# Kernel optimization log

Measured on AMD Instinct MI355X. Metric: run time of the kernel, lower is better.

Reference implementation:

```python
import jax, jax.numpy as jnp
import numpy as np

OUT_FEAT = 11008
IN_FEAT = 4096
HAD_DIM = 128


def setup_inputs() -> dict:
    key = jax.random.key(0)
    k1, k2, k3 = jax.random.split(key, 3)
    inp = jax.random.normal(k1, (OUT_FEAT, IN_FEAT), dtype=jnp.float32) * 0.02
    # rotation matrices (Hadamard-like random orthogonal stand-ins, scaled)
    R_left = jax.random.normal(k2, (IN_FEAT, IN_FEAT), dtype=jnp.float32) / np.sqrt(IN_FEAT)
    R_right = jax.random.normal(k3, (HAD_DIM, HAD_DIM), dtype=jnp.float32) / np.sqrt(HAD_DIM)
    return {"inp": inp, "R_left": R_left, "R_right": R_right}


def _fake_quant_int8(x):
    # symmetric per-tensor int8 fake quant with straight-through estimator
    scale = jnp.max(jnp.abs(x)) / 127.0
    scale = jnp.maximum(scale, jnp.finfo(x.dtype).tiny)
    q = jnp.clip(jnp.round(x / scale), -127.0, 127.0) * scale
    return x + jax.lax.stop_gradient(q - x)


def reference(inp, R_left, R_right):
    # RotQuantWrapper.forward, branch: R_left is not None, R1_is_left=True, R_right set.
    org_dtype = inp.dtype
    out_feat, in_feat = inp.shape  # inp is W^T: (out_feat, in_feat)
    compute_dtype = jnp.float32
    # inp @ R_left  -> (out_feat, in_feat)
    x = inp.astype(compute_dtype) @ R_left.astype(compute_dtype)
    had_dim = R_right.shape[0]
    # (W^T A)^T -> reshape -> block-multiply by B (had_dim blocks) -> back
    x = x.T  # (in_feat, out_feat)
    x = x.reshape(in_feat, out_feat // had_dim, had_dim)
    x = x @ R_right.astype(compute_dtype)  # batched small matmul over 128-blocks
    x = x.reshape(in_feat, out_feat).T  # (out_feat, in_feat)
    x = x.astype(org_dtype)
    return _fake_quant_int8(x)
```

## Files before the change

kernel.cpp:

```cpp
#include <hip/hip_runtime.h>

#define OUT_FEAT 11008
#define IN_FEAT  4096
#define HAD      128

typedef __attribute__((ext_vector_type(8))) _Float16 f16x8;
typedef __attribute__((ext_vector_type(4))) float    f32x4;

__device__ __forceinline__ void lds_load16(const _Float16* g, _Float16* l) {
    __builtin_amdgcn_global_load_lds(
        (const __attribute__((address_space(1))) void*)g,
        (__attribute__((address_space(3))) void*)l, 16, 0, 0);
}

__global__ void k_transpose_convert(const float* __restrict__ Rl, _Float16* __restrict__ Bt) {
    __shared__ float tile[64][65];
    int n0 = blockIdx.x * 64;
    int k0 = blockIdx.y * 64;
    int t  = threadIdx.x;
    int tn = t & 63;
    int tr = t >> 6;
#pragma unroll
    for (int r = 0; r < 16; ++r) {
        int kk = r * 4 + tr;
        tile[kk][tn] = Rl[(size_t)(k0 + kk) * IN_FEAT + n0 + tn];
    }
    __syncthreads();
#pragma unroll
    for (int r = 0; r < 16; ++r) {
        int nn = r * 4 + tr;
        Bt[(size_t)(n0 + nn) * IN_FEAT + k0 + tn] = (_Float16)tile[tn][nn];
    }
}

__global__ __launch_bounds__(256, 1) void k_rotate(const float* __restrict__ inp,
                                                   const float* __restrict__ Rr,
                                                   _Float16* __restrict__ W) {
    __shared__ float sR[HAD * HAD];
    __shared__ float sX[HAD * 128];
    int i0 = blockIdx.x * 128;
    int b  = blockIdx.y;
    int t  = threadIdx.x;

    for (int r = 0; r < 64; ++r) {
        int idx = r * 256 + t;
        sR[idx] = Rr[idx];
    }
    const float* xsrc = inp + (size_t)b * HAD * IN_FEAT + i0;
    for (int r = 0; r < 64; ++r) {
        int idx = r * 256 + t;
        int k = idx >> 7, ii = idx & 127;
        sX[idx] = xsrc[(size_t)k * IN_FEAT + ii];
    }
    __syncthreads();

    int tx = t & 15, ty = t >> 4;
    int j0 = ty * 8, ii0 = tx * 8;
    float acc[8][8];
#pragma unroll
    for (int a = 0; a < 8; ++a)
#pragma unroll
        for (int c = 0; c < 8; ++c) acc[a][c] = 0.f;

    for (int k = 0; k < 128; ++k) {
        float4 ra = *(const float4*)&sR[k * 128 + j0];
        float4 rb = *(const float4*)&sR[k * 128 + j0 + 4];
        float4 xa = *(const float4*)&sX[k * 128 + ii0];
        float4 xb = *(const float4*)&sX[k * 128 + ii0 + 4];
        float rv[8] = {ra.x, ra.y, ra.z, ra.w, rb.x, rb.y, rb.z, rb.w};
        float xv[8] = {xa.x, xa.y, xa.z, xa.w, xb.x, xb.y, xb.z, xb.w};
#pragma unroll
        for (int jj = 0; jj < 8; ++jj)
#pragma unroll
            for (int ii = 0; ii < 8; ++ii)
                acc[jj][ii] = fmaf(rv[jj], xv[ii], acc[jj][ii]);
    }

#pragma unroll
    for (int jj = 0; jj < 8; ++jj) {
        f16x8 v;
#pragma unroll
        for (int ii = 0; ii < 8; ++ii) v[ii] = (_Float16)acc[jj][ii];
        *(f16x8*)&W[(size_t)(b * HAD + j0 + jj) * IN_FEAT + i0 + ii0] = v;
    }
}

#define BM 256
#define BN 256
#define BK 32
#define NT (IN_FEAT / BK)

__global__ __launch_bounds__(512, 2) void k_gemm(const _Float16* __restrict__ A,
                                                 const _Float16* __restrict__ B,
                                                 float* __restrict__ C,
                                                 unsigned* __restrict__ absmax) {
    __shared__ _Float16 sA[4][BM * BK];
    __shared__ _Float16 sB[4][BN * BK];

    int obid = blockIdx.x;
    int cpx  = 688 >> 3;
    int bid  = (obid & 7) * cpx + (obid >> 3);
    int m0 = (bid >> 4) * BM;
    int n0 = (bid & 15) * BN;

    int t    = threadIdx.x;
    int lane = t & 63;
    int wid  = t >> 6;
    int wr   = wid >> 2;
    int wc   = wid & 3;

    int pc0 = t;
    int pc1 = t + 512;
    int rowP0 = pc0 >> 2, rowP1 = pc1 >> 2;
    int csw0 = ((pc0 & 3) ^ ((pc0 >> 3) & 3)) * 8;
    int csw1 = ((pc1 & 3) ^ ((pc1 >> 3) & 3)) * 8;
    const _Float16* A0 = A + (size_t)(m0 + rowP0) * IN_FEAT + csw0;
    const _Float16* A1 = A + (size_t)(m0 + rowP1) * IN_FEAT + csw1;
    const _Float16* B0 = B + (size_t)(n0 + rowP0) * IN_FEAT + csw0;
    const _Float16* B1 = B + (size_t)(n0 + rowP1) * IN_FEAT + csw1;
    int ldsOff0 = (wid * 64) * 8;
    int ldsOff1 = (512 + wid * 64) * 8;

    auto stageA = [&](int s, int kt) {
        lds_load16(A0 + kt * BK, &sA[s][ldsOff0]);
        lds_load16(A1 + kt * BK, &sA[s][ldsOff1]);
    };
    auto stageB = [&](int s, int kt) {
        lds_load16(B0 + kt * BK, &sB[s][ldsOff0]);
        lds_load16(B1 + kt * BK, &sB[s][ldsOff1]);
    };

    int fr  = lane & 15;
    int fc8 = (((lane >> 4) ^ ((lane >> 1) & 3))) * 8;
    int aoff0 = (wr * 128 + fr) * BK + fc8;
    int aoff1 = (wr * 128 + 64 + fr) * BK + fc8;
    int boff  = (wc * 64 + fr) * BK + fc8;

    f32x4 acc[8][4] = {};
    f16x8 af[4], bf[4];

    stageA(0, 0); stageB(0, 0);
    stageA(1, 1); stageB(1, 1);
    asm volatile("s_waitcnt vmcnt(4)" ::: "memory");
    __builtin_amdgcn_s_barrier();

    for (int kt = 0; kt < NT; ++kt) {
        int s  = kt & 3;
        int sn = (kt + 2) & 3;
        bool st = (kt + 2) < NT;

        const _Float16* pa = &sA[s][aoff0];
        const _Float16* pb = &sB[s][boff];
#pragma unroll
        for (int i = 0; i < 4; ++i) bf[i] = *(const f16x8*)(pb + i * 16 * BK);
#pragma unroll
        for (int i = 0; i < 4; ++i) af[i] = *(const f16x8*)(pa + i * 16 * BK);
        if (st) stageA(sn, kt + 2);
        __builtin_amdgcn_s_barrier();
        __builtin_amdgcn_s_setprio(1);
#pragma unroll
        for (int mi = 0; mi < 4; ++mi)
#pragma unroll
            for (int ni = 0; ni < 4; ++ni)
                acc[mi][ni] = __builtin_amdgcn_mfma_f32_16x16x32_f16(af[mi], bf[ni], acc[mi][ni], 0, 0, 0);
        __builtin_amdgcn_s_setprio(0);
        __builtin_amdgcn_s_barrier();

        const _Float16* pa1 = &sA[s][aoff1];
#pragma unroll
        for (int i = 0; i < 4; ++i) af[i] = *(const f16x8*)(pa1 + i * 16 * BK);
        if (st) stageB(sn, kt + 2);
        __builtin_amdgcn_s_barrier();
        __builtin_amdgcn_s_setprio(1);
#pragma unroll
        for (int mi = 0; mi < 4; ++mi)
#pragma unroll
            for (int ni = 0; ni < 4; ++ni)
                acc[4 + mi][ni] = __builtin_amdgcn_mfma_f32_16x16x32_f16(af[mi], bf[ni], acc[4 + mi][ni], 0, 0, 0);
        __builtin_amdgcn_s_setprio(0);
        if (st) asm volatile("s_waitcnt vmcnt(4)" ::: "memory");
        else    asm volatile("s_waitcnt vmcnt(0)" ::: "memory");
        __builtin_amdgcn_s_barrier();
    }

    float mx = 0.f;
#pragma unroll
    for (int mi = 0; mi < 8; ++mi)
#pragma unroll
        for (int ni = 0; ni < 4; ++ni)
#pragma unroll
            for (int r = 0; r < 4; ++r) mx = fmaxf(mx, fabsf(acc[mi][ni][r]));
#pragma unroll
    for (int off = 32; off; off >>= 1) mx = fmaxf(mx, __shfl_xor(mx, off));
    if (lane == 0) atomicMax(absmax, __float_as_uint(mx));

#pragma unroll
    for (int mi = 0; mi < 8; ++mi) {
        int row_base = m0 + wr * 128 + mi * 16 + (lane >> 4) * 4;
#pragma unroll
        for (int ni = 0; ni < 4; ++ni) {
            int col = n0 + wc * 64 + ni * 16 + (lane & 15);
#pragma unroll
            for (int r = 0; r < 4; ++r)
                C[(size_t)(row_base + r) * IN_FEAT + col] = acc[mi][ni][r];
        }
    }
}

__global__ void k_quant(float* __restrict__ C, const unsigned* __restrict__ absmax, int n4) {
    int i = blockIdx.x * blockDim.x + threadIdx.x;
    if (i >= n4) return;
    float amax  = __uint_as_float(*absmax);
    float scale = fmaxf(amax / 127.0f, 1.17549435e-38f);
    float4 v = ((const float4*)C)[i];
    float4 o;
    o.x = fminf(127.f, fmaxf(-127.f, rintf(v.x / scale))) * scale;
    o.y = fminf(127.f, fmaxf(-127.f, rintf(v.y / scale))) * scale;
    o.z = fminf(127.f, fmaxf(-127.f, rintf(v.z / scale))) * scale;
    o.w = fminf(127.f, fmaxf(-127.f, rintf(v.w / scale))) * scale;
    ((float4*)C)[i] = o;
}

extern "C" void kernel_launch(void* const* d_in, const int* in_sizes, int n_in,
                              void* d_out, int out_size, void* d_ws, size_t ws_size,
                              hipStream_t stream) {
    const float* inp = (const float*)d_in[0];
    const float* Rl  = (const float*)d_in[1];
    const float* Rr  = (const float*)d_in[2];
    float* out = (float*)d_out;

    char* ws = (char*)d_ws;
    const size_t W_BYTES  = (size_t)OUT_FEAT * IN_FEAT * 2;
    const size_t BT_BYTES = (size_t)IN_FEAT * IN_FEAT * 2;
    _Float16* Wh   = (_Float16*)ws;
    _Float16* Bt   = (_Float16*)(ws + W_BYTES);
    unsigned* amax = (unsigned*)(ws + W_BYTES + BT_BYTES);

    hipMemsetAsync(amax, 0, 4, stream);
    k_transpose_convert<<<dim3(IN_FEAT / 64, IN_FEAT / 64), 256, 0, stream>>>(Rl, Bt);
    k_rotate<<<dim3(IN_FEAT / 128, OUT_FEAT / HAD), 256, 0, stream>>>(inp, Rr, Wh);
    k_gemm<<<dim3((OUT_FEAT / BM) * (IN_FEAT / BN)), 512, 0, stream>>>(Wh, Bt, out, amax);
    int n4 = OUT_FEAT * IN_FEAT / 4;
    k_quant<<<(n4 + 255) / 256, 256, 0, stream>>>(out, amax, n4);
}
```

Measured before the change: 699.3 us.

## Restructure GEMM main loop to BK=64 with half-tile staged double buffering

Raises the GEMM K-tile from 32 to 64 and splits each A/B tile into 128-row halves staged separately into LDS. The loop becomes four MFMA phases per K-step, each interleaved with one half-tile async load. Loads are ordered A one step ahead and B two steps ahead, with a new XOR swizzle for 64-wide rows. The aim is to halve loop iterations and barriers per unit of work and to overlap global-to-LDS traffic with MFMA better. In exchange it adds more barriers per iteration and tighter buffer-reuse hazards, and LDS use stays at 128KB per block.

```diff
diff --git a/kernel.cpp b/kernel.cpp
--- a/kernel.cpp
+++ b/kernel.cpp
@@ -87,99 +87,125 @@
 
 #define BM 256
 #define BN 256
-#define BK 32
+#define BK 64
 #define NT (IN_FEAT / BK)
 
 __global__ __launch_bounds__(512, 2) void k_gemm(const _Float16* __restrict__ A,
                                                  const _Float16* __restrict__ B,
                                                  float* __restrict__ C,
                                                  unsigned* __restrict__ absmax) {
-    __shared__ _Float16 sA[4][BM * BK];
-    __shared__ _Float16 sB[4][BN * BK];
+    __shared__ _Float16 sA[4 * 8192];
+    __shared__ _Float16 sB[4 * 8192];
 
     int obid = blockIdx.x;
-    int cpx  = 688 >> 3;
-    int bid  = (obid & 7) * cpx + (obid >> 3);
+    int bid  = (obid & 7) * 86 + (obid >> 3);
     int m0 = (bid >> 4) * BM;
     int n0 = (bid & 15) * BN;
 
-    int t    = threadIdx.x;
-    int lane = t & 63;
-    int wid  = t >> 6;
-    int wr   = wid >> 2;
-    int wc   = wid & 3;
-
-    int pc0 = t;
-    int pc1 = t + 512;
-    int rowP0 = pc0 >> 2, rowP1 = pc1 >> 2;
-    int csw0 = ((pc0 & 3) ^ ((pc0 >> 3) & 3)) * 8;
-    int csw1 = ((pc1 & 3) ^ ((pc1 >> 3) & 3)) * 8;
-    const _Float16* A0 = A + (size_t)(m0 + rowP0) * IN_FEAT + csw0;
-    const _Float16* A1 = A + (size_t)(m0 + rowP1) * IN_FEAT + csw1;
-    const _Float16* B0 = B + (size_t)(n0 + rowP0) * IN_FEAT + csw0;
-    const _Float16* B1 = B + (size_t)(n0 + rowP1) * IN_FEAT + csw1;
-    int ldsOff0 = (wid * 64) * 8;
-    int ldsOff1 = (512 + wid * 64) * 8;
-
-    auto stageA = [&](int s, int kt) {
-        lds_load16(A0 + kt * BK, &sA[s][ldsOff0]);
-        lds_load16(A1 + kt * BK, &sA[s][ldsOff1]);
+    int t = threadIdx.x, lane = t & 63, wid = t >> 6;
+    int wr = wid >> 2, wc = wid & 3;
+    int fr = lane & 15, g = lane >> 4;
+
+    int r0 = t >> 3,        r1 = (t + 512) >> 3;
+    int cs0 = ((t & 7) ^ (r0 & 7)) * 8;
+    int cs1 = (((t + 512) & 7) ^ (r1 & 7)) * 8;
+    size_t sOff0 = (size_t)r0 * IN_FEAT + cs0;
+    size_t sOff1 = (size_t)r1 * IN_FEAT + cs1;
+    const _Float16* Abase = A + (size_t)m0 * IN_FEAT;
+    const _Float16* Bbase = B + (size_t)n0 * IN_FEAT;
+    int d0 = (wid * 64) * 8;
+    int d1 = (512 + wid * 64) * 8;
+
+    auto stA = [&](int bufi, int h, int ktc) {
+        const _Float16* s = Abase + (size_t)(h * 128) * IN_FEAT + ktc * BK;
+        _Float16* d = &sA[(bufi * 2 + h) * 8192];
+        lds_load16(s + sOff0, d + d0);
+        lds_load16(s + sOff1, d + d1);
     };
-    auto stageB = [&](int s, int kt) {
-        lds_load16(B0 + kt * BK, &sB[s][ldsOff0]);
-        lds_load16(B1 + kt * BK, &sB[s][ldsOff1]);
+    auto stB = [&](int bufi, int h, int ktc) {
+        const _Float16* s = Bbase + (size_t)(h * 128) * IN_FEAT + ktc * BK;
+        _Float16* d = &sB[(bufi * 2 + h) * 8192];
+        lds_load16(s + sOff0, d + d0);
+        lds_load16(s + sOff1, d + d1);
     };
 
-    int fr  = lane & 15;
-    int fc8 = (((lane >> 4) ^ ((lane >> 1) & 3))) * 8;
-    int aoff0 = (wr * 128 + fr) * BK + fc8;
-    int aoff1 = (wr * 128 + 64 + fr) * BK + fc8;
-    int boff  = (wc * 64 + fr) * BK + fc8;
+    int pk0 = ((g) ^ (fr & 7)) * 8;
+    int pk1 = (((4 | g)) ^ (fr & 7)) * 8;
+    int aRow = fr * 64;
+    int bRow = (wc & 1) * 4096 + fr * 64;
 
     f32x4 acc[8][4] = {};
-    f16x8 af[4], bf[4];
-
-    stageA(0, 0); stageB(0, 0);
-    stageA(1, 1); stageB(1, 1);
+    f16x8 a[4], b0[4], b1[4];
+
+    stB(0, 0, 0); stB(0, 1, 0);
+    stA(0, 0, 0); stA(0, 1, 0);
+    stB(1, 0, 1); stB(1, 1, 1);
     asm volatile("s_waitcnt vmcnt(4)" ::: "memory");
     __builtin_amdgcn_s_barrier();
 
     for (int kt = 0; kt < NT; ++kt) {
-        int s  = kt & 3;
-        int sn = (kt + 2) & 3;
-        bool st = (kt + 2) < NT;
-
-        const _Float16* pa = &sA[s][aoff0];
-        const _Float16* pb = &sB[s][boff];
-#pragma unroll
-        for (int i = 0; i < 4; ++i) bf[i] = *(const f16x8*)(pb + i * 16 * BK);
-#pragma unroll
-        for (int i = 0; i < 4; ++i) af[i] = *(const f16x8*)(pa + i * 16 * BK);
-        if (st) stageA(sn, kt + 2);
-        __builtin_amdgcn_s_barrier();
-        __builtin_amdgcn_s_setprio(1);
-#pragma unroll
-        for (int mi = 0; mi < 4; ++mi)
-#pragma unroll
-            for (int ni = 0; ni < 4; ++ni)
-                acc[mi][ni] = __builtin_amdgcn_mfma_f32_16x16x32_f16(af[mi], bf[ni], acc[mi][ni], 0, 0, 0);
-        __builtin_amdgcn_s_setprio(0);
-        __builtin_amdgcn_s_barrier();
-
-        const _Float16* pa1 = &sA[s][aoff1];
-#pragma unroll
-        for (int i = 0; i < 4; ++i) af[i] = *(const f16x8*)(pa1 + i * 16 * BK);
-        if (st) stageB(sn, kt + 2);
-        __builtin_amdgcn_s_barrier();
-        __builtin_amdgcn_s_setprio(1);
-#pragma unroll
-        for (int mi = 0; mi < 4; ++mi)
-#pragma unroll
-            for (int ni = 0; ni < 4; ++ni)
-                acc[4 + mi][ni] = __builtin_amdgcn_mfma_f32_16x16x32_f16(af[mi], bf[ni], acc[4 + mi][ni], 0, 0, 0);
-        __builtin_amdgcn_s_setprio(0);
-        if (st) asm volatile("s_waitcnt vmcnt(4)" ::: "memory");
-        else    asm volatile("s_waitcnt vmcnt(0)" ::: "memory");
+        int buf = kt & 1, nb = buf ^ 1;
+        const _Float16* sa = &sA[(buf * 2 + wr) * 8192 + aRow];
+        const _Float16* sb = &sB[(buf * 2 + (wc >> 1)) * 8192 + bRow];
+        bool ok1 = (kt + 1) < NT;
+        bool ok2 = (kt + 2) < NT;
+
+#pragma unroll
+        for (int i = 0; i < 4; ++i) a[i]  = *(const f16x8*)(sa + i * 1024 + pk0);
+#pragma unroll
+        for (int i = 0; i < 4; ++i) b0[i] = *(const f16x8*)(sb + i * 1024 + pk0);
+        if (ok1) stA(nb, 0, kt + 1);
+        __builtin_amdgcn_s_barrier();
+        __builtin_amdgcn_s_setprio(1);
+#pragma unroll
+        for (int mi = 0; mi < 4; ++mi)
+#pragma unroll
+            for (int ni = 0; ni < 4; ++ni)
+                acc[mi][ni] = __builtin_amdgcn_mfma_f32_16x16x32_f16(a[mi], b0[ni], acc[mi][ni], 0, 0, 0);
+        __builtin_amdgcn_s_setprio(0);
+        __builtin_amdgcn_s_barrier();
+
+#pragma unroll
+        for (int i = 0; i < 4; ++i) a[i]  = *(const f16x8*)(sa + i * 1024 + pk1);
+#pragma unroll
+        for (int i = 0; i < 4; ++i) b1[i] = *(const f16x8*)(sb + i * 1024 + pk1);
+        if (ok1) stA(nb, 1, kt + 1);
+        __builtin_amdgcn_s_barrier();
+        __builtin_amdgcn_s_setprio(1);
+#pragma unroll
+        for (int mi = 0; mi < 4; ++mi)
+#pragma unroll
+            for (int ni = 0; ni < 4; ++ni)
+                acc[mi][ni] = __builtin_amdgcn_mfma_f32_16x16x32_f16(a[mi], b1[ni], acc[mi][ni], 0, 0, 0);
+        __builtin_amdgcn_s_setprio(0);
+        __builtin_amdgcn_s_barrier();
+
+#pragma unroll
+        for (int i = 0; i < 4; ++i) a[i] = *(const f16x8*)(sa + (4 + i) * 1024 + pk0);
+        if (ok2) stB(buf, 0, kt + 2);
+        __builtin_amdgcn_s_barrier();
+        __builtin_amdgcn_s_setprio(1);
+#pragma unroll
+        for (int mi = 0; mi < 4; ++mi)
+#pragma unroll
+            for (int ni = 0; ni < 4; ++ni)
+                acc[4 + mi][ni] = __builtin_amdgcn_mfma_f32_16x16x32_f16(a[mi], b0[ni], acc[4 + mi][ni], 0, 0, 0);
+        __builtin_amdgcn_s_setprio(0);
+        __builtin_amdgcn_s_barrier();
+
+#pragma unroll
+        for (int i = 0; i < 4; ++i) a[i] = *(const f16x8*)(sa + (4 + i) * 1024 + pk1);
+        if (ok2) stB(buf, 1, kt + 2);
+        __builtin_amdgcn_s_barrier();
+        __builtin_amdgcn_s_setprio(1);
+#pragma unroll
+        for (int mi = 0; mi < 4; ++mi)
+#pragma unroll
+            for (int ni = 0; ni < 4; ++ni)
+                acc[4 + mi][ni] = __builtin_amdgcn_mfma_f32_16x16x32_f16(a[mi], b1[ni], acc[4 + mi][ni], 0, 0, 0);
+        __builtin_amdgcn_s_setprio(0);
+        if (ok2) asm volatile("s_waitcnt vmcnt(4)" ::: "memory");
+        else     asm volatile("s_waitcnt vmcnt(0)" ::: "memory");
         __builtin_amdgcn_s_barrier();
     }
 
```

Result: slower. 717.9 us (+2.7%).
